# Kernel tuning notes

Hardware: AMD Instinct MI355X
Metric: run time of the kernel (lower is better)

Reference implementation:

```python
import jax, jax.numpy as jnp
import numpy as np

B, S, E = 1, 2048, 2048
H = 16            # num_q_heads
DN = 128          # qk_nope_head_dim
DR = 64           # qk_rope_head_dim
DV = 128          # v_head_dim
R = 512           # kv_lora_rank
QLR = 1536        # q_lora_rank
EPS = 1e-6
ROPE_BASE = 10000.0


def _rmsnorm(x, w):
    var = jnp.mean(jnp.square(x), axis=-1, keepdims=True)
    return x * jax.lax.rsqrt(var + EPS) * w


def _rope_cos_sin(seqlen):
    inv_freq = 1.0 / (ROPE_BASE ** (jnp.arange(0, DR, 2, dtype=jnp.float32) / DR))
    ang = jnp.arange(seqlen, dtype=jnp.float32)[:, None] * inv_freq[None, :]  # [S, DR/2]
    cos = jnp.concatenate([jnp.cos(ang), jnp.cos(ang)], axis=-1)  # [S, DR]
    sin = jnp.concatenate([jnp.sin(ang), jnp.sin(ang)], axis=-1)
    return cos, sin


def _rotate_half(x):
    x1, x2 = jnp.split(x, 2, axis=-1)
    return jnp.concatenate([-x2, x1], axis=-1)


def setup_inputs() -> dict:
    key = jax.random.key(0)
    ks = jax.random.split(key, 8)
    sd = lambda fan_in: 1.0 / np.sqrt(fan_in)
    return {
        "x": jax.random.normal(ks[0], (B, S, E), jnp.float32),
        "w_q_a": jax.random.normal(ks[1], (E, QLR), jnp.float32) * sd(E),
        "q_a_ln_w": jnp.ones((QLR,), jnp.float32),
        "w_q_b": jax.random.normal(ks[2], (QLR, H * (DN + DR)), jnp.float32) * sd(QLR),
        "w_kv_a": jax.random.normal(ks[3], (E, R + DR), jnp.float32) * sd(E),
        "kv_a_ln_w": jnp.ones((R,), jnp.float32),
        "w_kv_b": jax.random.normal(ks[4], (R, H * (DN + DV)), jnp.float32) * sd(R),
        "w_o": jax.random.normal(ks[5], (H * DV, E), jnp.float32) * sd(H * DV),
    }


def reference(x, w_q_a, q_a_ln_w, w_q_b, w_kv_a, kv_a_ln_w, w_kv_b, w_o):
    b, s, _ = x.shape
    # --- low-rank query projection: q_a -> RMSNorm -> q_b ---
    q_a = _rmsnorm(x @ w_q_a, q_a_ln_w)                      # [b,s,QLR]
    q = (q_a @ w_q_b).reshape(b, s, H, DN + DR)               # [b,s,H,192]
    q_nope, q_pe = q[..., :DN], q[..., DN:]
    # --- compressed KV projection (MQA, single KV head) ---
    ckv_kpe = x @ w_kv_a                                      # [b,s,R+DR]
    ckv = _rmsnorm(ckv_kpe[..., :R], kv_a_ln_w)               # [b,s,R]
    k_pe = ckv_kpe[..., R:].reshape(b, s, 1, DR)              # [b,s,1,DR]
    # --- partial RoPE on the rope sub-dims only ---
    cos, sin = _rope_cos_sin(s)
    cos, sin = cos[None, :, None, :], sin[None, :, None, :]
    q_pe = q_pe * cos + _rotate_half(q_pe) * sin
    k_pe = k_pe * cos + _rotate_half(k_pe) * sin
    # --- weight absorption: fold W_uk into q, W_uv @ W_o into output ---
    w_kv = w_kv_b.reshape(R, H, DN + DV)
    w_uk = w_kv[..., :DN]                                     # [R,H,DN]
    w_uv = w_kv[..., DN:]                                     # [R,H,DV]
    w_o3 = w_o.reshape(H, DV, E)
    w_o_abs = jnp.einsum('rhd,hde->hre', w_uv, w_o3)          # [H,R,E]
    q_abs = jnp.einsum('bshd,rhd->bshr', q_nope, w_uk)        # [b,s,H,R]
    # --- attention in compressed (ckv + rope) space ---
    q_full = jnp.concatenate([q_abs, q_pe], axis=-1)          # [b,s,H,R+DR]
    k_full = jnp.concatenate([ckv, k_pe[:, :, 0, :]], axis=-1)  # [b,s,R+DR]
    sm_scale = (DN + DR) ** -0.5
    scores = jnp.einsum('bqhd,bkd->bhqk', q_full, k_full) * sm_scale
    causal = jnp.tril(jnp.ones((s, s), dtype=bool))
    scores = jnp.where(causal[None, None], scores, jnp.finfo(scores.dtype).min)
    attn = jax.nn.softmax(scores, axis=-1)
    o_ckv = jnp.einsum('bhqk,bkr->bqhr', attn, ckv)           # [b,s,H,R]
    # --- absorbed output projection, summed over heads ---
    y = jnp.einsum('bqhr,hre->bqe', o_ckv, w_o_abs)           # [b,s,E]
    return y
```

## Files before the change

kernel.cpp:

```cpp
#include <hip/hip_runtime.h>
#include <math.h>


typedef unsigned short u16;
typedef unsigned int u32;
typedef __bf16 bf16x8 __attribute__((ext_vector_type(8)));
typedef float f32x4 __attribute__((ext_vector_type(4)));
typedef unsigned short u16x8 __attribute__((ext_vector_type(8)));

__device__ __forceinline__ u16 f2b(float f) {
  u32 u = __float_as_uint(f);
  u += 0x7FFFu + ((u >> 16) & 1u);
  return (u16)(u >> 16);
}
__device__ __forceinline__ float b2f(u16 v) {
  return __uint_as_float(((u32)v) << 16);
}

#define GLDS(g, l) __builtin_amdgcn_global_load_lds( \
    (const __attribute__((address_space(1))) u32*)(g), \
    (__attribute__((address_space(3))) u32*)(l), 16, 0, 0)

#define MFMA(a, b, c) __builtin_amdgcn_mfma_f32_16x16x32_bf16(a, b, c, 0, 0, 0)

template<int N>
__device__ __forceinline__ void vm_barrier() {
  __builtin_amdgcn_s_waitcnt(0xF70 | N);
  __builtin_amdgcn_s_barrier();
}

#define N_ITEMS 1280
__device__ __forceinline__ int nkc_of(int qt) { return (((qt >> 1) + 1) + 3) >> 2; }

__device__ __forceinline__ float block_sum(float v, float* red) {
#pragma unroll
  for (int off = 32; off > 0; off >>= 1) v += __shfl_down(v, off);
  const int lane = threadIdx.x & 63, w = threadIdx.x >> 6;
  if (lane == 0) red[w] = v;
  __syncthreads();
  float r = red[0] + red[1] + red[2] + red[3];
  __syncthreads();
  return r;
}

template<int OUTK>
__global__ __launch_bounds__(256) void gemm_mfma(
    const u16* __restrict__ A, const u16* __restrict__ B, void* __restrict__ Cv,
    int K, int lda, int ldb, int ldc, long sA, long sB, long sC)
{
  __shared__ u16 At[3][4096];
  __shared__ u16 Bt[3][4096];
  const u16* Ab = A + (long)blockIdx.z * sA;
  const u16* Bb = B + (long)blockIdx.z * sB;
  const int tid = threadIdx.x;
  const int w = tid >> 6, lane = tid & 63;
  const int m0 = blockIdx.y * 128, n0 = blockIdx.x * 128;
  const int wm = (w >> 1) * 64, wn = (w & 1) * 64;
  const int fr = lane & 15, fq = lane >> 4;

  const int c0 = w * 2, c1 = w * 2 + 1;
  const int e0 = (c0 * 64 + lane) * 8, e1 = (c1 * 64 + lane) * 8;
  const int r0 = e0 >> 5, col0 = e0 & 31;
  const int r1 = e1 >> 5, col1 = e1 & 31;

  const int nk = K >> 5;
  auto issue = [&](int kc) {
    const int k0 = kc * 32;
    u16* at = At[kc % 3];
    u16* bt = Bt[kc % 3];
    GLDS(Ab + (long)(m0 + r0) * lda + k0 + col0, at + c0 * 512);
    GLDS(Bb + (long)(n0 + r0) * ldb + k0 + col0, bt + c0 * 512);
    GLDS(Ab + (long)(m0 + r1) * lda + k0 + col1, at + c1 * 512);
    GLDS(Bb + (long)(n0 + r1) * ldb + k0 + col1, bt + c1 * 512);
  };

  f32x4 acc[4][4] = {};
  issue(0);
  issue(1);
  vm_barrier<4>();
  for (int kc = 0; kc < nk; ++kc) {
    if (kc + 2 < nk) issue(kc + 2);
    const u16* at = At[kc % 3];
    const u16* bt = Bt[kc % 3];
    bf16x8 af[4], bfr[4];
#pragma unroll
    for (int i = 0; i < 4; ++i)
      af[i] = *(const bf16x8*)(at + (wm + i * 16 + fr) * 32 + fq * 8);
#pragma unroll
    for (int j = 0; j < 4; ++j)
      bfr[j] = *(const bf16x8*)(bt + (wn + j * 16 + fr) * 32 + fq * 8);
#pragma unroll
    for (int i = 0; i < 4; ++i)
#pragma unroll
      for (int j = 0; j < 4; ++j)
        acc[i][j] = MFMA(af[i], bfr[j], acc[i][j]);
    if (kc + 1 < nk) {
      if (kc + 2 < nk) vm_barrier<4>();
      else vm_barrier<0>();
    }
  }

  if (OUTK == 0) {
    float* C = (float*)Cv + (long)blockIdx.z * sC;
#pragma unroll
    for (int i = 0; i < 4; ++i)
#pragma unroll
      for (int j = 0; j < 4; ++j) {
        long base = (long)(m0 + wm + i * 16 + fq * 4) * ldc + (n0 + wn + j * 16 + fr);
#pragma unroll
        for (int r = 0; r < 4; ++r) C[base + (long)r * ldc] = acc[i][j][r];
      }
  } else if (OUTK == 1) {
    u16* C = (u16*)Cv + (long)blockIdx.z * sC;
#pragma unroll
    for (int i = 0; i < 4; ++i)
#pragma unroll
      for (int j = 0; j < 4; ++j) {
        long base = (long)(m0 + wm + i * 16 + fq * 4) * ldc + (n0 + wn + j * 16 + fr);
#pragma unroll
        for (int r = 0; r < 4; ++r) C[base + (long)r * ldc] = f2b(acc[i][j][r]);
      }
  } else {
    u16* C = (u16*)Cv + (long)blockIdx.z * sC;
#pragma unroll
    for (int i = 0; i < 4; ++i)
#pragma unroll
      for (int j = 0; j < 4; ++j) {
        ushort4 v = { f2b(acc[i][j][0]), f2b(acc[i][j][1]),
                      f2b(acc[i][j][2]), f2b(acc[i][j][3]) };
        *(ushort4*)(C + (long)(n0 + wn + j * 16 + fr) * ldc + (m0 + wm + i * 16 + fq * 4)) = v;
      }
  }
}

__global__ void init_ctr(u32* ctr) { *ctr = 0; }

__global__ __launch_bounds__(256, 2) void attn_partial(
    const u16* __restrict__ qfb,
    const u16* __restrict__ kfb,
    const u16* __restrict__ vallT,
    u32* __restrict__ ctr,
    u16* __restrict__ pO,
    float* __restrict__ pS)
{
  __shared__ u16 Ks[3][4096];
  __shared__ u16 Vs[16384];
  __shared__ u16 Ps[4 * 2176];
  __shared__ u32 cur;

  const int tid = threadIdx.x;
  const int w = tid >> 6, lane = tid & 63;
  const int fr = lane & 15, fq = lane >> 4;
  const float scale = 0.07216878364870323f;
  u16* Psw = Ps + w * 2176;

  const int krow0 = (w * 2) * 16 + (lane >> 2);
  const int krow1 = (w * 2 + 1) * 16 + (lane >> 2);
  const int kg0 = (lane & 3) ^ (krow0 & 3);
  const int kg1 = (lane & 3) ^ (krow1 & 3);
  const int vlanecol = lane >> 4;
  const int vslot = lane & 15;

  while (true) {
    if (tid == 0) cur = atomicAdd(ctr, 1u);
    __syncthreads();
    const u32 it = cur;
    if (it >= N_ITEMS) break;

    int rem = (int)it, qt = 31, kc = 0, h = 0;
    for (int q = 31; q >= 0; --q) {
      int cnt = nkc_of(q) * 16;
      if (rem < cnt) { qt = q; kc = rem >> 4; h = rem & 15; break; }
      rem -= cnt;
    }
    const int q0 = qt * 64;
    const int ktt = (qt >> 1) + 1;
    const int kt0 = kc * 4, kt1 = min(kt0 + 4, ktt);

    bf16x8 aq[18];
    {
      const u16* qp = qfb + (long)(q0 + w * 16 + fr) * 9216 + h * 576 + fq * 8;
#pragma unroll
      for (int d = 0; d < 18; ++d) aq[d] = *(const bf16x8*)(qp + d * 32);
    }

    float m_run[4], l_run[4];
#pragma unroll
    for (int r = 0; r < 4; ++r) { m_run[r] = -1e30f; l_run[r] = 0.f; }
    f32x4 Oacc[8] = {};
    const u16* vbase = vallT + (long)h * 262144;

    for (int kt = kt0; kt < kt1; ++kt) {
      const int k0 = kt * 128;
      auto issueK = [&](int c) {
        const int d0 = c * 32;
        u16* dst = Ks[c % 3];
        GLDS(kfb + (long)(k0 + krow0) * 576 + d0 + kg0 * 8, dst + (w * 2) * 512);
        GLDS(kfb + (long)(k0 + krow1) * 576 + d0 + kg1 * 8, dst + (w * 2 + 1) * 512);
      };

      issueK(0);
      issueK(1);
      vm_barrier<2>();
      f32x4 sc[8] = {};
#pragma unroll
      for (int d = 0; d < 18; ++d) {
        if (d + 2 < 18) issueK(d + 2);
        const u16* kb = Ks[d % 3];
#pragma unroll
        for (int j = 0; j < 8; ++j) {
          const int row = j * 16 + fr;
          bf16x8 b = *(const bf16x8*)(kb + row * 32 + ((fq ^ (row & 3)) * 8));
          sc[j] = MFMA(aq[d], b, sc[j]);
        }
        if (d < 17) {
          if (d + 2 < 18) vm_barrier<2>();
          else vm_barrier<0>();
        }
      }

#pragma unroll
      for (int c = 0; c < 8; ++c) {
        const int i = w * 8 + c;
        const int vcol = i * 4 + vlanecol;
        const int g = vslot ^ (vcol & 15);
        GLDS(vbase + (long)vcol * 2048 + k0 + g * 8, Vs + i * 512);
      }

      const bool diag = (kt == ktt - 1);
#pragma unroll
      for (int r = 0; r < 4; ++r) {
        float mx = m_run[r];
#pragma unroll
        for (int j = 0; j < 8; ++j) {
          float s = sc[j][r] * scale;
          if (diag) {
            const int row = q0 + w * 16 + fq * 4 + r;
            const int col = k0 + j * 16 + fr;
            if (col > row) s = -1e30f;
          }
          sc[j][r] = s;
          mx = fmaxf(mx, s);
        }
        mx = fmaxf(mx, __shfl_xor(mx, 1));
        mx = fmaxf(mx, __shfl_xor(mx, 2));
        mx = fmaxf(mx, __shfl_xor(mx, 4));
        mx = fmaxf(mx, __shfl_xor(mx, 8));
        const float alpha = __expf(m_run[r] - mx);
        m_run[r] = mx;
        float sum = 0.f;
#pragma unroll
        for (int j = 0; j < 8; ++j) {
          float p = __expf(sc[j][r] - mx);
          sc[j][r] = p;
          sum += p;
        }
        sum += __shfl_xor(sum, 1);
        sum += __shfl_xor(sum, 2);
        sum += __shfl_xor(sum, 4);
        sum += __shfl_xor(sum, 8);
        l_run[r] = l_run[r] * alpha + sum;
#pragma unroll
        for (int jv = 0; jv < 8; ++jv) Oacc[jv][r] *= alpha;
#pragma unroll
        for (int j = 0; j < 8; ++j)
          Psw[(fq * 4 + r) * 136 + j * 16 + fr] = f2b(sc[j][r]);
      }
      vm_barrier<0>();

#pragma unroll
      for (int ks = 0; ks < 4; ++ks) {
        bf16x8 ap = *(const bf16x8*)(Psw + fr * 136 + ks * 32 + fq * 8);
#pragma unroll
        for (int jv = 0; jv < 8; ++jv) {
          const int vcol = jv * 16 + fr;
          bf16x8 vb = *(const bf16x8*)(Vs + vcol * 128 + (((ks * 4 + fq) ^ fr) * 8));
          Oacc[jv] = MFMA(ap, vb, Oacc[jv]);
        }
      }
      __builtin_amdgcn_s_barrier();
    }

    const long po = (long)it * 8192;
#pragma unroll
    for (int r = 0; r < 4; ++r) {
      const int lr = w * 16 + fq * 4 + r;
      if (fr == 0) {
        pS[((long)it * 64 + lr) * 2] = m_run[r];
        pS[((long)it * 64 + lr) * 2 + 1] = l_run[r];
      }
#pragma unroll
      for (int jv = 0; jv < 8; ++jv)
        pO[po + (long)lr * 128 + jv * 16 + fr] = f2b(Oacc[jv][r]);
    }
  }
}

__global__ __launch_bounds__(256) void attn_reduce(
    const u16* __restrict__ pO, const float* __restrict__ pS,
    u16* __restrict__ ovb)
{
  const int h = blockIdx.x, qt = blockIdx.y;
  const int ktt = (qt >> 1) + 1;
  const int nkc = (ktt + 3) >> 2;
  int base = 0;
  for (int q = qt + 1; q < 32; ++q) base += nkc_of(q) * 16;
  const int tid = threadIdx.x;
  const int r = tid >> 2, cq = (tid & 3) * 32;

  float m[4], l[4], wgt[4];
  float M = -1e30f;
  for (int i = 0; i < nkc; ++i) {
    const long slot = base + i * 16 + h;
    m[i] = pS[(slot * 64 + r) * 2];
    l[i] = pS[(slot * 64 + r) * 2 + 1];
    M = fmaxf(M, m[i]);
  }
  float L = 0.f;
  for (int i = 0; i < nkc; ++i) { wgt[i] = __expf(m[i] - M); L += l[i] * wgt[i]; }
  const float inv = 1.0f / L;

  u16* orow = ovb + (long)(qt * 64 + r) * 2048 + h * 128 + cq;
  for (int c8 = 0; c8 < 32; c8 += 8) {
    float acc[8] = {};
    for (int i = 0; i < nkc; ++i) {
      const u16x8 v = *(const u16x8*)(pO + ((long)(base + i * 16 + h) * 64 + r) * 128 + cq + c8);
#pragma unroll
      for (int e = 0; e < 8; ++e) acc[e] += b2f(v[e]) * wgt[i];
    }
    u16x8 o;
#pragma unroll
    for (int e = 0; e < 8; ++e) o[e] = f2b(acc[e] * inv);
    *(u16x8*)(orow + c8) = o;
  }
}

__global__ __launch_bounds__(256) void cast_bf16(const float* __restrict__ in,
                                                 u16* __restrict__ out, long n) {
  long i = ((long)blockIdx.x * 256 + threadIdx.x) * 4;
  if (i >= n) return;
  float4 v = *(const float4*)(in + i);
  ushort4 o = { f2b(v.x), f2b(v.y), f2b(v.z), f2b(v.w) };
  *(ushort4*)(out + i) = o;
}

__global__ __launch_bounds__(256) void transpose_cast(const float* __restrict__ in,
    u16* __restrict__ out, int ldi, int ldo, long sIn, long sOut) {
  in += (long)blockIdx.z * sIn;
  out += (long)blockIdx.z * sOut;
  __shared__ u16 t[32][33];
  const int i0 = blockIdx.y * 32, j0 = blockIdx.x * 32;
  const int tx = threadIdx.x & 31, ty = threadIdx.x >> 5;
  for (int r = ty; r < 32; r += 8)
    t[r][tx] = f2b(in[(long)(i0 + r) * ldi + j0 + tx]);
  __syncthreads();
  for (int r = ty; r < 32; r += 8)
    out[(long)(j0 + r) * ldo + i0 + tx] = t[tx][r];
}

__global__ __launch_bounds__(256) void rmsnorm_cast(const float* __restrict__ in,
    const float* __restrict__ w, u16* __restrict__ out, int n, int ldin) {
  __shared__ float red[4];
  const float* row = in + (long)blockIdx.x * ldin;
  u16* orow = out + (long)blockIdx.x * n;
  float ss = 0.f;
  for (int i = threadIdx.x; i < n; i += 256) { float v = row[i]; ss += v * v; }
  float tot = block_sum(ss, red);
  float inv = rsqrtf(tot / (float)n + 1e-6f);
  for (int i = threadIdx.x; i < n; i += 256) orow[i] = f2b(row[i] * inv * w[i]);
}

__global__ __launch_bounds__(256) void rope_table(float* tab) {
  int s = blockIdx.x * 8 + (threadIdx.x >> 5), j = threadIdx.x & 31;
  double freq = pow(10000.0, -(double)j / 32.0);
  double ang = (double)s * freq;
  tab[s * 64 + j] = (float)cos(ang);
  tab[s * 64 + 32 + j] = (float)sin(ang);
}

__global__ __launch_bounds__(256) void build_kfull(const float* __restrict__ ckv,
    const float* __restrict__ lnw, const float* __restrict__ tab, u16* __restrict__ kfb) {
  __shared__ float red[4];
  const int s = blockIdx.x;
  const float* row = ckv + (long)s * 2176;
  float ss = 0.f;
  for (int i = threadIdx.x; i < 512; i += 256) { float v = row[i]; ss += v * v; }
  float tot = block_sum(ss, red);
  float inv = rsqrtf(tot / 512.0f + 1e-6f);
  u16* orow = kfb + (long)s * 576;
  for (int i = threadIdx.x; i < 512; i += 256) orow[i] = f2b(row[i] * inv * lnw[i]);
  if (threadIdx.x < 64) {
    int i = threadIdx.x, j = i & 31;
    float c = tab[s * 64 + j], sn = tab[s * 64 + 32 + j];
    float xv = row[512 + i];
    float rot = (i < 32) ? -row[512 + i + 32] : row[512 + i - 32];
    orow[512 + i] = f2b(xv * c + rot * sn);
  }
}

__global__ __launch_bounds__(256) void rope_qpe(const u16* __restrict__ qb,
    const float* __restrict__ tab, u16* __restrict__ qfb) {
  const int s = blockIdx.x;
  const int h = threadIdx.x >> 4;
  const int i0 = (threadIdx.x & 15) * 4;
  const u16* src = qb + (long)s * 3072 + h * 192 + 128;
  u16* dst = qfb + (long)s * 9216 + h * 576 + 512;
#pragma unroll
  for (int k = 0; k < 4; ++k) {
    const int i = i0 + k, j = i & 31;
    float c = tab[s * 64 + j], sn = tab[s * 64 + 32 + j];
    float xv = b2f(src[i]);
    float rot = (i < 32) ? -b2f(src[i + 32]) : b2f(src[i - 32]);
    dst[i] = f2b(xv * c + rot * sn);
  }
}

extern "C" void kernel_launch(void* const* d_in, const int* in_sizes, int n_in,
                              void* d_out, int out_size, void* d_ws, size_t ws_size,
                              hipStream_t stream) {
  const float* x      = (const float*)d_in[0];
  const float* w_q_a  = (const float*)d_in[1];
  const float* q_ln   = (const float*)d_in[2];
  const float* w_q_b  = (const float*)d_in[3];
  const float* w_kv_a = (const float*)d_in[4];
  const float* kv_ln  = (const float*)d_in[5];
  const float* w_kv_b = (const float*)d_in[6];
  const float* w_o    = (const float*)d_in[7];
  float* out = (float*)d_out;

  char* p = (char*)d_ws;
  float* tab   = (float*)p;  p += 524288;
  u16* wkvbb   = (u16*)p;    p += 4194304;
  u16* wuvT    = (u16*)p;    p += 2097152;
  u16* woT     = (u16*)p;    p += 8388608;
  u16* qfb     = (u16*)p;    p += 37748736;
  u16* vallT   = (u16*)p;    p += 8388608;
  u16* kfb     = (u16*)p;    p += 2359296;
  u16* ovb     = (u16*)p;    p += 8388608;
  char* tb = p;
  u16* xb      = (u16*)tb;
  u16* wabT    = (u16*)(tb + 8388608);
  float* qac   = (float*)(tb + 17301504);
  u16* qab     = (u16*)(tb + 35127296);
  u16* wqbT    = (u16*)(tb + 41418752);
  u16* qb      = (u16*)(tb + 50855936);
  u16* pO      = (u16*)tb;
  float* pS    = (float*)(tb + 20971520);
  u32* ctr     = (u32*)(tb + 21626880);

  rope_table<<<dim3(256), 256, 0, stream>>>(tab);

  cast_bf16<<<4096, 256, 0, stream>>>(x, xb, 4194304);
  transpose_cast<<<dim3(48, 64), 256, 0, stream>>>(w_q_a, wabT, 1536, 2048, 0, 0);
  transpose_cast<<<dim3(18, 64), 256, 0, stream>>>(w_kv_a, wabT + 1536 * 2048, 576, 2048, 0, 0);
  transpose_cast<<<dim3(96, 48), 256, 0, stream>>>(w_q_b, wqbT, 3072, 1536, 0, 0);
  cast_bf16<<<2048, 256, 0, stream>>>(w_kv_b, wkvbb, 2097152);
  transpose_cast<<<dim3(4, 16, 16), 256, 0, stream>>>(w_kv_b + 128, wuvT, 4096, 512, 256, 65536);
  transpose_cast<<<dim3(64, 64), 256, 0, stream>>>(w_o, woT, 2048, 2048, 0, 0);

  gemm_mfma<0><<<dim3(17, 16), 256, 0, stream>>>(
      xb, wabT, qac, 2048, 2048, 2048, 2176, 0, 0, 0);
  rmsnorm_cast<<<2048, 256, 0, stream>>>(qac, q_ln, qab, 1536, 2176);
  build_kfull<<<2048, 256, 0, stream>>>(qac + 1536, kv_ln, tab, kfb);

  gemm_mfma<1><<<dim3(24, 16), 256, 0, stream>>>(
      qab, wqbT, qb, 1536, 1536, 1536, 3072, 0, 0, 0);

  gemm_mfma<1><<<dim3(4, 16, 16), 256, 0, stream>>>(
      qb, wkvbb, qfb, 128, 3072, 4096, 9216, 192, 256, 576);
  rope_qpe<<<dim3(2048), 256, 0, stream>>>(qb, tab, qfb);

  gemm_mfma<2><<<dim3(1, 16, 16), 256, 0, stream>>>(
      kfb, wuvT, vallT, 512, 576, 512, 2048, 0, 65536, 262144);

  init_ctr<<<1, 1, 0, stream>>>(ctr);
  attn_partial<<<dim3(512), 256, 0, stream>>>(qfb, kfb, vallT, ctr, pO, pS);
  attn_reduce<<<dim3(16, 32), 256, 0, stream>>>(pO, pS, ovb);

  gemm_mfma<0><<<dim3(16, 16), 256, 0, stream>>>(
      ovb, woT, out, 2048, 2048, 2048, 2048, 0, 0, 0);
}
```

Before: 476.3 us.

## Load V directly to registers, prefetch next K tile, raise attention occupancy

```diff
diff --git a/kernel.cpp b/kernel.cpp
--- a/kernel.cpp
+++ b/kernel.cpp
@@ -135,7 +135,7 @@
 
 __global__ void init_ctr(u32* ctr) { *ctr = 0; }
 
-__global__ __launch_bounds__(256, 2) void attn_partial(
+__global__ __launch_bounds__(256, 3) void attn_partial(
     const u16* __restrict__ qfb,
     const u16* __restrict__ kfb,
     const u16* __restrict__ vallT,
@@ -144,7 +144,6 @@
     float* __restrict__ pS)
 {
   __shared__ u16 Ks[3][4096];
-  __shared__ u16 Vs[16384];
   __shared__ u16 Ps[4 * 2176];
   __shared__ u32 cur;
 
@@ -158,8 +157,6 @@
   const int krow1 = (w * 2 + 1) * 16 + (lane >> 2);
   const int kg0 = (lane & 3) ^ (krow0 & 3);
   const int kg1 = (lane & 3) ^ (krow1 & 3);
-  const int vlanecol = lane >> 4;
-  const int vslot = lane & 15;
 
   while (true) {
     if (tid == 0) cur = atomicAdd(ctr, 1u);
@@ -188,44 +185,50 @@
 #pragma unroll
     for (int r = 0; r < 4; ++r) { m_run[r] = -1e30f; l_run[r] = 0.f; }
     f32x4 Oacc[8] = {};
-    const u16* vbase = vallT + (long)h * 262144;
+    const u16* vlane = vallT + (long)h * 262144 + (long)fr * 2048 + fq * 8;
+
+    auto issueK = [&](int kt, int c) {
+      const int k0i = kt * 128, d0 = c * 32;
+      u16* dst = Ks[c % 3];
+      GLDS(kfb + (long)(k0i + krow0) * 576 + d0 + kg0 * 8, dst + (w * 2) * 512);
+      GLDS(kfb + (long)(k0i + krow1) * 576 + d0 + kg1 * 8, dst + (w * 2 + 1) * 512);
+    };
+
+    issueK(kt0, 0);
+    issueK(kt0, 1);
 
     for (int kt = kt0; kt < kt1; ++kt) {
       const int k0 = kt * 128;
-      auto issueK = [&](int c) {
-        const int d0 = c * 32;
-        u16* dst = Ks[c % 3];
-        GLDS(kfb + (long)(k0 + krow0) * 576 + d0 + kg0 * 8, dst + (w * 2) * 512);
-        GLDS(kfb + (long)(k0 + krow1) * 576 + d0 + kg1 * 8, dst + (w * 2 + 1) * 512);
-      };
-
-      issueK(0);
-      issueK(1);
       vm_barrier<2>();
+
       f32x4 sc[8] = {};
 #pragma unroll
       for (int d = 0; d < 18; ++d) {
-        if (d + 2 < 18) issueK(d + 2);
+        if (d + 2 < 18) issueK(kt, d + 2);
         const u16* kb = Ks[d % 3];
+        __builtin_amdgcn_s_setprio(1);
 #pragma unroll
         for (int j = 0; j < 8; ++j) {
           const int row = j * 16 + fr;
           bf16x8 b = *(const bf16x8*)(kb + row * 32 + ((fq ^ (row & 3)) * 8));
           sc[j] = MFMA(aq[d], b, sc[j]);
         }
+        __builtin_amdgcn_s_setprio(0);
         if (d < 17) {
           if (d + 2 < 18) vm_barrier<2>();
           else vm_barrier<0>();
         }
       }
-
-#pragma unroll
-      for (int c = 0; c < 8; ++c) {
-        const int i = w * 8 + c;
-        const int vcol = i * 4 + vlanecol;
-        const int g = vslot ^ (vcol & 15);
-        GLDS(vbase + (long)vcol * 2048 + k0 + g * 8, Vs + i * 512);
-      }
+      __builtin_amdgcn_s_barrier();
+
+      const u16* vk = vlane + k0;
+      bf16x8 vA[4], vB[4];
+#pragma unroll
+      for (int q = 0; q < 4; ++q) {
+        vA[q] = *(const bf16x8*)(vk + (long)q * 32768);
+        vB[q] = *(const bf16x8*)(vk + (long)(q + 4) * 32768);
+      }
+      if (kt + 1 < kt1) { issueK(kt + 1, 0); issueK(kt + 1, 1); }
 
       const bool diag = (kt == ktt - 1);
 #pragma unroll
@@ -266,19 +269,29 @@
         for (int j = 0; j < 8; ++j)
           Psw[(fq * 4 + r) * 136 + j * 16 + fr] = f2b(sc[j][r]);
       }
-      vm_barrier<0>();
 
 #pragma unroll
       for (int ks = 0; ks < 4; ++ks) {
         bf16x8 ap = *(const bf16x8*)(Psw + fr * 136 + ks * 32 + fq * 8);
-#pragma unroll
-        for (int jv = 0; jv < 8; ++jv) {
-          const int vcol = jv * 16 + fr;
-          bf16x8 vb = *(const bf16x8*)(Vs + vcol * 128 + (((ks * 4 + fq) ^ fr) * 8));
-          Oacc[jv] = MFMA(ap, vb, Oacc[jv]);
-        }
-      }
-      __builtin_amdgcn_s_barrier();
+        __builtin_amdgcn_s_setprio(1);
+#pragma unroll
+        for (int q = 0; q < 4; ++q) Oacc[q] = MFMA(ap, vA[q], Oacc[q]);
+        __builtin_amdgcn_s_setprio(0);
+        if (ks < 3) {
+#pragma unroll
+          for (int q = 0; q < 4; ++q)
+            vA[q] = *(const bf16x8*)(vk + (long)q * 32768 + (ks + 1) * 32);
+        }
+        __builtin_amdgcn_s_setprio(1);
+#pragma unroll
+        for (int q = 0; q < 4; ++q) Oacc[q + 4] = MFMA(ap, vB[q], Oacc[q + 4]);
+        __builtin_amdgcn_s_setprio(0);
+        if (ks < 3) {
+#pragma unroll
+          for (int q = 0; q < 4; ++q)
+            vB[q] = *(const bf16x8*)(vk + (long)(q + 4) * 32768 + (ks + 1) * 32);
+        }
+      }
     }
 
     const long po = (long)it * 8192;
@@ -474,7 +487,7 @@
       kfb, wuvT, vallT, 512, 576, 512, 2048, 0, 65536, 262144);
 
   init_ctr<<<1, 1, 0, stream>>>(ctr);
-  attn_partial<<<dim3(512), 256, 0, stream>>>(qfb, kfb, vallT, ctr, pO, pS);
+  attn_partial<<<dim3(768), 256, 0, stream>>>(qfb, kfb, vallT, ctr, pO, pS);
   attn_reduce<<<dim3(16, 32), 256, 0, stream>>>(pO, pS, ovb);
 
   gemm_mfma<0><<<dim3(16, 16), 256, 0, stream>>>(
```

Result: slower. 606.4 us (+27.3%).
